# Optimization experiments

Measured on AMD Instinct MI355X. Metric: run time of the kernel, lower is better.

## Reference

```python
import jax, jax.numpy as jnp
import numpy as np

N_NODES = 16384
HID_IN = 1024   # hid_size (GCN in/out dim)
HID_MID = 1500  # hidden_size
N_EDGES = 131072


def setup_inputs() -> dict:
    key = jax.random.key(0)
    k1, k2, k3, k4, k5, k6 = jax.random.split(key, 6)
    x = jax.random.normal(k1, (N_NODES, HID_IN), dtype=jnp.float32)
    edge_index = jax.random.randint(k2, (2, N_EDGES), 0, N_NODES, dtype=jnp.int64)
    # GCNConv weights (glorot-ish scale) and biases
    W1 = jax.random.normal(k3, (HID_IN, HID_MID), dtype=jnp.float32) / np.sqrt(HID_IN)
    b1 = jnp.zeros((HID_MID,), dtype=jnp.float32)
    W2 = jax.random.normal(k4, (HID_MID, HID_IN), dtype=jnp.float32) / np.sqrt(HID_MID)
    b2 = jnp.zeros((HID_IN,), dtype=jnp.float32)
    return {"x": x, "edge_index": edge_index, "W1": W1, "b1": b1, "W2": W2, "b2": b2}


def _gcn_conv(x, W, b, src, dst, inv_sqrt_deg, n_nodes):
    # PyG GCNConv: out[i] = sum_{(j->i)} d_j^{-1/2} d_i^{-1/2} (x W)[j] + b
    h = x @ W                                   # [N, out]
    norm = inv_sqrt_deg[src] * inv_sqrt_deg[dst]  # [E]
    msg = h[src] * norm[:, None]                 # gather + scale [E, out]
    out = jax.ops.segment_sum(msg, dst, num_segments=n_nodes)
    return out + b


def reference(x, edge_index, W1, b1, W2, b2):
    n = x.shape[0]
    # add self-loops (GCNConv default)
    loops = jnp.arange(n, dtype=edge_index.dtype)
    src = jnp.concatenate([edge_index[0], loops])
    dst = jnp.concatenate([edge_index[1], loops])
    deg = jax.ops.segment_sum(jnp.ones_like(dst, dtype=x.dtype), dst, num_segments=n)
    inv_sqrt_deg = jnp.where(deg > 0, jax.lax.rsqrt(jnp.maximum(deg, 1.0)), 0.0)
    h = _gcn_conv(x, W1, b1, src, dst, inv_sqrt_deg, n)
    h = jax.nn.relu(h)  # dropout skipped (eval mode)
    out = _gcn_conv(h, W2, b2, src, dst, inv_sqrt_deg, n)
    return out
```

## Files before the change

### kernel.cpp

```cpp
#include <hip/hip_runtime.h>
#include <cstdint>
#include <cstddef>

#define NN 16384
#define DIN 1024
#define DMID 1500
#define DMIDP 1536
#define NE 131072

typedef __bf16 bf16;
typedef __bf16 bf16x4 __attribute__((ext_vector_type(4)));
typedef __bf16 bf16x8 __attribute__((ext_vector_type(8)));
typedef float f32x4 __attribute__((ext_vector_type(4)));

#define GLOBAL_AS __attribute__((address_space(1)))
#define LDS_AS __attribute__((address_space(3)))

__device__ __forceinline__ void gload_lds16(const bf16* g, bf16* l) {
    __builtin_amdgcn_global_load_lds((GLOBAL_AS const unsigned int*)(g),
                                     (LDS_AS unsigned int*)(l), 16, 0, 0);
}

#define SBAR() asm volatile("s_barrier" ::: "memory")
#define WAITV_(N) asm volatile("s_waitcnt vmcnt(" #N ")" ::: "memory")
#define WAITV(N) WAITV_(N)
#define WAITL0() asm volatile("s_waitcnt lgkmcnt(0)" ::: "memory")

__global__ void k_zero_cnt(int* cnt) {
    cnt[blockIdx.x * 256 + threadIdx.x] = 0;
}

__global__ void k_count(const int* __restrict__ dst, int* cnt) {
    int e = blockIdx.x * 256 + threadIdx.x;
    atomicAdd(&cnt[dst[e]], 1);
}

__global__ __launch_bounds__(1024) void k_scan(const int* __restrict__ cnt,
                                               int* __restrict__ rowptr,
                                               int* __restrict__ cursor,
                                               float* __restrict__ isd) {
    __shared__ int sums[1024];
    int t = threadIdx.x;
    int base = t * 16;
    int v[16], p[16];
    int s = 0;
#pragma unroll
    for (int k = 0; k < 16; ++k) {
        v[k] = cnt[base + k];
        p[k] = (v[k] + 7) & ~7;
        s += p[k];
    }
    sums[t] = s;
    __syncthreads();
    for (int off = 1; off < 1024; off <<= 1) {
        int y = (t >= off) ? sums[t - off] : 0;
        __syncthreads();
        sums[t] += y;
        __syncthreads();
    }
    int run = sums[t] - s;
#pragma unroll
    for (int k = 0; k < 16; ++k) {
        rowptr[base + k] = run;
        cursor[base + k] = run;
        isd[base + k] = rsqrtf((float)(v[k] + 1));
        run += p[k];
    }
    if (t == 1023) rowptr[NN] = run;
}

__global__ void k_fill(const int* __restrict__ src, const int* __restrict__ dst,
                       int* cursor, const float* __restrict__ isd,
                       int* __restrict__ csr_src, float* __restrict__ csr_w) {
    int e = blockIdx.x * 256 + threadIdx.x;
    int s = src[e], d = dst[e];
    int pos = atomicAdd(&cursor[d], 1);
    csr_src[pos] = s;
    csr_w[pos] = isd[s] * isd[d];
}

__global__ void k_pad(const int* __restrict__ cnt, const int* __restrict__ rowptr,
                      int* __restrict__ csr_src, float* __restrict__ csr_w) {
    int i = blockIdx.x * 256 + threadIdx.x;
    int c = cnt[i];
    int p = (c + 7) & ~7;
    int base = rowptr[i];
    for (int q = c; q < p; ++q) {
        csr_src[base + q] = i;
        csr_w[base + q] = 0.0f;
    }
}

__global__ void k_cvt_x(const float4* __restrict__ x, bf16x4* __restrict__ xb) {
    int i = blockIdx.x * 256 + threadIdx.x;
    float4 v = x[i];
    bf16x4 o;
    o[0] = (bf16)v.x; o[1] = (bf16)v.y; o[2] = (bf16)v.z; o[3] = (bf16)v.w;
    xb[i] = o;
}

__global__ void k_cvt_w1(const float* __restrict__ W1, bf16* __restrict__ W1b) {
    int n = blockIdx.x;
    for (int k = threadIdx.x; k < DIN; k += 256)
        W1b[n * DIN + k] = (n < DMID) ? (bf16)W1[(size_t)k * DMID + n] : (bf16)0.0f;
}

__global__ void k_cvt_w2(const float* __restrict__ W2, bf16* __restrict__ W2b) {
    int n = blockIdx.x;
    for (int k = threadIdx.x; k < DMIDP; k += 256)
        W2b[n * DMIDP + k] = (k < DMID) ? (bf16)W2[(size_t)k * DIN + n] : (bf16)0.0f;
}

template <int K, int N, bool RELU_BIAS>
__global__ __launch_bounds__(512, 2) void gemm256(const bf16* __restrict__ A,
                                                  const bf16* __restrict__ Bt,
                                                  bf16* __restrict__ C,
                                                  const float* __restrict__ bias) {
    constexpr int NT = K / 64;
    __shared__ __align__(16) bf16 lds[2][2][256 * 64];
    const int tid = threadIdx.x;
    const int w = tid >> 6;
    const int lane = tid & 63;
    const int bm = blockIdx.x, bn = blockIdx.y;
    const int fr = lane & 15, fq = lane >> 4;
    const int wm = w >> 2;
    const int wn = w & 3;
    const int sx = fr & 7;

    const int lrow = lane >> 3;
    const int lslot = (lane & 7) ^ lrow;
    const bf16* gA = A + (size_t)(bm * 256 + w * 8 + lrow) * K + lslot * 8;
    const bf16* gB = Bt + (size_t)(bn * 256 + w * 8 + lrow) * K + lslot * 8;

    f32x4 acc[8][4];
#pragma unroll
    for (int i = 0; i < 8; ++i)
#pragma unroll
        for (int j = 0; j < 4; ++j) acc[i][j] = {0.f, 0.f, 0.f, 0.f};

#define STAGE(T, BUF)                                                          \
    do {                                                                       \
        const bf16* _ga = gA + (size_t)(T) * 64;                               \
        const bf16* _gb = gB + (size_t)(T) * 64;                               \
        bf16* _la = &lds[BUF][0][0] + w * 512;                                 \
        bf16* _lb = &lds[BUF][1][0] + w * 512;                                 \
        _Pragma("unroll") for (int r = 0; r < 4; ++r)                          \
            gload_lds16(_ga + (size_t)r * (64 * K), _la + r * 4096);           \
        _Pragma("unroll") for (int r = 0; r < 4; ++r)                          \
            gload_lds16(_gb + (size_t)r * (64 * K), _lb + r * 4096);           \
    } while (0)

#define LDA4(DST, BUF, MH, KS)                                                 \
    _Pragma("unroll") for (int mt = 0; mt < 4; ++mt) {                         \
        int row = wm * 128 + (MH) * 64 + mt * 16 + fr;                         \
        int sl = (((KS) << 2) | fq) ^ sx;                                      \
        DST[mt] = *(const bf16x8*)((const char*)&lds[BUF][0][0] +              \
                                   row * 128 + sl * 16);                       \
    }
#define LDB4(DST, BUF, KS)                                                     \
    _Pragma("unroll") for (int nt = 0; nt < 4; ++nt) {                         \
        int row = wn * 64 + nt * 16 + fr;                                      \
        int sl = (((KS) << 2) | fq) ^ sx;                                      \
        DST[nt] = *(const bf16x8*)((const char*)&lds[BUF][1][0] +              \
                                   row * 128 + sl * 16);                       \
    }
#define MFMA16(MH, AF, BF)                                                     \
    __builtin_amdgcn_s_setprio(1);                                             \
    _Pragma("unroll") for (int mt = 0; mt < 4; ++mt)                           \
    _Pragma("unroll") for (int nt = 0; nt < 4; ++nt)                           \
        acc[(MH) * 4 + mt][nt] = __builtin_amdgcn_mfma_f32_16x16x32_bf16(      \
            AF[mt], BF[nt], acc[(MH) * 4 + mt][nt], 0, 0, 0);                  \
    __builtin_amdgcn_s_setprio(0);

    bf16x8 a0[4], a1[4], b0[4], b1[4];

    STAGE(0, 0);
    STAGE(1, 1);
    WAITV(8);
    SBAR();
    LDA4(a0, 0, 0, 0);
    LDB4(b0, 0, 0);

    for (int t = 0; t < NT; ++t) {
        const int b = t & 1;
        LDA4(a1, b, 1, 0);
        MFMA16(0, a0, b0);
        LDA4(a0, b, 0, 1);
        LDB4(b1, b, 1);
        MFMA16(1, a1, b0);
        LDA4(a1, b, 1, 1);
        MFMA16(0, a0, b1);
        if (t + 1 < NT) {
            WAITL0();
            WAITV(0);
            SBAR();
            if (t + 2 < NT) STAGE(t + 2, b);
            LDA4(a0, b ^ 1, 0, 0);
            LDB4(b0, b ^ 1, 0);
        }
        MFMA16(1, a1, b1);
    }
#undef STAGE
#undef LDA4
#undef LDB4
#undef MFMA16

    float bv[4];
    if (RELU_BIAS) {
#pragma unroll
        for (int nt = 0; nt < 4; ++nt) {
            int col = bn * 256 + wn * 64 + nt * 16 + fr;
            bv[nt] = (col < DMID) ? bias[col] : 0.0f;
        }
    }
#pragma unroll
    for (int mq = 0; mq < 8; ++mq) {
        int row0 = bm * 256 + wm * 128 + mq * 16 + fq * 4;
#pragma unroll
        for (int nt = 0; nt < 4; ++nt) {
            int col = bn * 256 + wn * 64 + nt * 16 + fr;
#pragma unroll
            for (int r = 0; r < 4; ++r) {
                float v = acc[mq][nt][r];
                if (RELU_BIAS) v = fmaxf(v + bv[nt], 0.0f);
                C[(size_t)(row0 + r) * N + col] = (bf16)v;
            }
        }
    }
}

__global__ __launch_bounds__(128) void k_aggX(const bf16* __restrict__ X,
                                              const int* __restrict__ rowptr,
                                              const int* __restrict__ csr_src,
                                              const float* __restrict__ csr_w,
                                              const float* __restrict__ isd,
                                              bf16* __restrict__ XA) {
    int i = blockIdx.x;
    int t = threadIdx.x;
    int c0 = t * 8;
    int beg = rowptr[i], end = rowptr[i + 1];
    float wi = isd[i];
    float w0 = wi * wi;
    float a[8];
    bf16x8 h = *(const bf16x8*)&X[(size_t)i * DIN + c0];
#pragma unroll
    for (int k = 0; k < 8; ++k) a[k] = w0 * (float)h[k];
    for (int e = beg; e < end; e += 8) {
        int j[8];
        float w[8];
        bf16x8 hv[8];
#pragma unroll
        for (int q = 0; q < 8; ++q) { j[q] = csr_src[e + q]; w[q] = csr_w[e + q]; }
#pragma unroll
        for (int q = 0; q < 8; ++q)
            hv[q] = *(const bf16x8*)&X[(size_t)j[q] * DIN + c0];
#pragma unroll
        for (int q = 0; q < 8; ++q)
#pragma unroll
            for (int k = 0; k < 8; ++k) a[k] += w[q] * (float)hv[q][k];
    }
    bf16x8 o;
#pragma unroll
    for (int k = 0; k < 8; ++k) o[k] = (bf16)a[k];
    *(bf16x8*)&XA[(size_t)i * DIN + c0] = o;
}

__global__ __launch_bounds__(128) void k_agg2(const bf16* __restrict__ H,
                                              const int* __restrict__ rowptr,
                                              const int* __restrict__ csr_src,
                                              const float* __restrict__ csr_w,
                                              const float* __restrict__ isd,
                                              const float* __restrict__ b2,
                                              float* __restrict__ out) {
    int i = blockIdx.x;
    int t = threadIdx.x;
    int c0 = t * 8;
    int beg = rowptr[i], end = rowptr[i + 1];
    float wi = isd[i];
    float w0 = wi * wi;
    float a[8];
    bf16x8 h = *(const bf16x8*)&H[(size_t)i * DIN + c0];
#pragma unroll
    for (int k = 0; k < 8; ++k) a[k] = w0 * (float)h[k];
    for (int e = beg; e < end; e += 8) {
        int j[8];
        float w[8];
        bf16x8 hv[8];
#pragma unroll
        for (int q = 0; q < 8; ++q) { j[q] = csr_src[e + q]; w[q] = csr_w[e + q]; }
#pragma unroll
        for (int q = 0; q < 8; ++q)
            hv[q] = *(const bf16x8*)&H[(size_t)j[q] * DIN + c0];
#pragma unroll
        for (int q = 0; q < 8; ++q)
#pragma unroll
            for (int k = 0; k < 8; ++k) a[k] += w[q] * (float)hv[q][k];
    }
    float4 o0, o1;
    o0.x = a[0] + b2[c0 + 0]; o0.y = a[1] + b2[c0 + 1];
    o0.z = a[2] + b2[c0 + 2]; o0.w = a[3] + b2[c0 + 3];
    o1.x = a[4] + b2[c0 + 4]; o1.y = a[5] + b2[c0 + 5];
    o1.z = a[6] + b2[c0 + 6]; o1.w = a[7] + b2[c0 + 7];
    *(float4*)&out[(size_t)i * DIN + c0] = o0;
    *(float4*)&out[(size_t)i * DIN + c0 + 4] = o1;
}

extern "C" void kernel_launch(void* const* d_in, const int* in_sizes, int n_in,
                              void* d_out, int out_size, void* d_ws, size_t ws_size,
                              hipStream_t stream) {
    const float* x = (const float*)d_in[0];
    const int* ei = (const int*)d_in[1];
    const float* W1 = (const float*)d_in[2];
    const float* b1 = (const float*)d_in[3];
    const float* W2 = (const float*)d_in[4];
    const float* b2 = (const float*)d_in[5];
    float* out = (float*)d_out;
    const int* src = ei;
    const int* dst = ei + NE;

    char* ws = (char*)d_ws;
    int* cnt      = (int*)(ws + 0);
    int* cursor   = (int*)(ws + 65536);
    float* isd    = (float*)(ws + 131072);
    int* rowptr   = (int*)(ws + 196608);
    int* csr_src  = (int*)(ws + 327680);
    float* csr_w  = (float*)(ws + 2424832);
    bf16* Xb      = (bf16*)(ws + 4521984);
    bf16* XA      = (bf16*)(ws + 38076416);
    bf16* W1b     = (bf16*)(ws + 71630848);
    bf16* W2b     = (bf16*)(ws + 74776576);
    bf16* Y1b     = (bf16*)(ws + 77922304);
    bf16* H2b     = XA;

    k_zero_cnt<<<NN / 256, 256, 0, stream>>>(cnt);
    k_count<<<NE / 256, 256, 0, stream>>>(dst, cnt);
    k_scan<<<1, 1024, 0, stream>>>(cnt, rowptr, cursor, isd);
    k_fill<<<NE / 256, 256, 0, stream>>>(src, dst, cursor, isd, csr_src, csr_w);
    k_pad<<<NN / 256, 256, 0, stream>>>(cnt, rowptr, csr_src, csr_w);

    k_cvt_x<<<NN * DIN / 4 / 256, 256, 0, stream>>>((const float4*)x, (bf16x4*)Xb);
    k_cvt_w1<<<DMIDP, 256, 0, stream>>>(W1, W1b);
    k_cvt_w2<<<DIN, 256, 0, stream>>>(W2, W2b);

    k_aggX<<<NN, 128, 0, stream>>>(Xb, rowptr, csr_src, csr_w, isd, XA);
    dim3 g1(NN / 256, DMIDP / 256);
    gemm256<DIN, DMIDP, true><<<g1, 512, 0, stream>>>(XA, W1b, Y1b, b1);

    dim3 g2(NN / 256, DIN / 256);
    gemm256<DMIDP, DIN, false><<<g2, 512, 0, stream>>>(Y1b, W2b, H2b, nullptr);
    k_agg2<<<NN, 128, 0, stream>>>(H2b, rowptr, csr_src, csr_w, isd, b2, out);
}
```

Before: 378.1 us.

## Parameterize GEMM M-tile, simplify K-loop, stage epilogue through LDS for vector stores

Templates the GEMM on M-tile size so the first GEMM uses 128-row tiles (more blocks for better CU fill) while the second keeps 256. The software-pipelined register double-buffering of fragments is replaced by a simpler per-k-step load-then-MFMA loop. The epilogue now writes accumulators into LDS and emits 16-byte coalesced global stores instead of scattered 2-byte stores. Risks are less LDS/MFMA overlap from the removed fragment prefetch and extra barriers in the epilogue.

Measured after the change: 509.5 us. 1.35x slower.

```diff
diff --git a/kernel.cpp b/kernel.cpp
--- a/kernel.cpp
+++ b/kernel.cpp
@@ -111,13 +111,19 @@
         W2b[n * DMIDP + k] = (k < DMID) ? (bf16)W2[(size_t)k * DIN + n] : (bf16)0.0f;
 }
 
-template <int K, int N, bool RELU_BIAS>
+template <int BM, int K, int N, bool RELU_BIAS>
 __global__ __launch_bounds__(512, 2) void gemm256(const bf16* __restrict__ A,
                                                   const bf16* __restrict__ Bt,
                                                   bf16* __restrict__ C,
                                                   const float* __restrict__ bias) {
+    static_assert(BM == 128 || BM == 256, "");
     constexpr int NT = K / 64;
-    __shared__ __align__(16) bf16 lds[2][2][256 * 64];
+    constexpr int WM = BM / 2;
+    constexpr int M_FR = WM / 16;
+    constexpr int AR = BM / 64;
+    constexpr int TOK = AR + 4;
+    __shared__ __align__(16) bf16 ldsA[2][BM * 64];
+    __shared__ __align__(16) bf16 ldsB[2][256 * 64];
     const int tid = threadIdx.x;
     const int w = tid >> 6;
     const int lane = tid & 63;
@@ -129,82 +135,74 @@
 
     const int lrow = lane >> 3;
     const int lslot = (lane & 7) ^ lrow;
-    const bf16* gA = A + (size_t)(bm * 256 + w * 8 + lrow) * K + lslot * 8;
-    const bf16* gB = Bt + (size_t)(bn * 256 + w * 8 + lrow) * K + lslot * 8;
-
-    f32x4 acc[8][4];
-#pragma unroll
-    for (int i = 0; i < 8; ++i)
+    const bf16* gA = A + (size_t)(bm * BM + w * 8 * AR + lrow) * K + lslot * 8;
+    const bf16* gB = Bt + (size_t)(bn * 256 + w * 32 + lrow) * K + lslot * 8;
+
+    f32x4 acc[M_FR][4];
+#pragma unroll
+    for (int i = 0; i < M_FR; ++i)
 #pragma unroll
         for (int j = 0; j < 4; ++j) acc[i][j] = {0.f, 0.f, 0.f, 0.f};
 
 #define STAGE(T, BUF)                                                          \
     do {                                                                       \
-        const bf16* _ga = gA + (size_t)(T) * 64;                               \
-        const bf16* _gb = gB + (size_t)(T) * 64;                               \
-        bf16* _la = &lds[BUF][0][0] + w * 512;                                 \
-        bf16* _lb = &lds[BUF][1][0] + w * 512;                                 \
+        _Pragma("unroll") for (int r = 0; r < AR; ++r)                         \
+            gload_lds16(gA + (size_t)(T) * 64 + (size_t)(r * 8) * K,           \
+                        &ldsA[BUF][0] + w * (AR * 512) + r * 512);             \
         _Pragma("unroll") for (int r = 0; r < 4; ++r)                          \
-            gload_lds16(_ga + (size_t)r * (64 * K), _la + r * 4096);           \
-        _Pragma("unroll") for (int r = 0; r < 4; ++r)                          \
-            gload_lds16(_gb + (size_t)r * (64 * K), _lb + r * 4096);           \
+            gload_lds16(gB + (size_t)(T) * 64 + (size_t)(r * 8) * K,           \
+                        &ldsB[BUF][0] + w * 2048 + r * 512);                   \
     } while (0)
-
-#define LDA4(DST, BUF, MH, KS)                                                 \
-    _Pragma("unroll") for (int mt = 0; mt < 4; ++mt) {                         \
-        int row = wm * 128 + (MH) * 64 + mt * 16 + fr;                         \
-        int sl = (((KS) << 2) | fq) ^ sx;                                      \
-        DST[mt] = *(const bf16x8*)((const char*)&lds[BUF][0][0] +              \
-                                   row * 128 + sl * 16);                       \
-    }
-#define LDB4(DST, BUF, KS)                                                     \
-    _Pragma("unroll") for (int nt = 0; nt < 4; ++nt) {                         \
-        int row = wn * 64 + nt * 16 + fr;                                      \
-        int sl = (((KS) << 2) | fq) ^ sx;                                      \
-        DST[nt] = *(const bf16x8*)((const char*)&lds[BUF][1][0] +              \
-                                   row * 128 + sl * 16);                       \
-    }
-#define MFMA16(MH, AF, BF)                                                     \
-    __builtin_amdgcn_s_setprio(1);                                             \
-    _Pragma("unroll") for (int mt = 0; mt < 4; ++mt)                           \
-    _Pragma("unroll") for (int nt = 0; nt < 4; ++nt)                           \
-        acc[(MH) * 4 + mt][nt] = __builtin_amdgcn_mfma_f32_16x16x32_bf16(      \
-            AF[mt], BF[nt], acc[(MH) * 4 + mt][nt], 0, 0, 0);                  \
-    __builtin_amdgcn_s_setprio(0);
-
-    bf16x8 a0[4], a1[4], b0[4], b1[4];
 
     STAGE(0, 0);
     STAGE(1, 1);
-    WAITV(8);
+    if constexpr (TOK == 6) { WAITV(6); } else { WAITV(8); }
     SBAR();
-    LDA4(a0, 0, 0, 0);
-    LDB4(b0, 0, 0);
 
     for (int t = 0; t < NT; ++t) {
-        const int b = t & 1;
-        LDA4(a1, b, 1, 0);
-        MFMA16(0, a0, b0);
-        LDA4(a0, b, 0, 1);
-        LDB4(b1, b, 1);
-        MFMA16(1, a1, b0);
-        LDA4(a1, b, 1, 1);
-        MFMA16(0, a0, b1);
+        const int c = t & 1;
+#pragma unroll
+        for (int ks = 0; ks < 2; ++ks) {
+            bf16x8 bq[4];
+#pragma unroll
+            for (int nt = 0; nt < 4; ++nt) {
+                int row = wn * 64 + nt * 16 + fr;
+                int sl = ((ks << 2) | fq) ^ sx;
+                bq[nt] = *(const bf16x8*)((const char*)&ldsB[c][0] +
+                                          row * 128 + sl * 16);
+            }
+#pragma unroll
+            for (int mh = 0; mh < M_FR / 4; ++mh) {
+                bf16x8 af[4];
+#pragma unroll
+                for (int mt = 0; mt < 4; ++mt) {
+                    int row = wm * WM + mh * 64 + mt * 16 + fr;
+                    int sl = ((ks << 2) | fq) ^ sx;
+                    af[mt] = *(const bf16x8*)((const char*)&ldsA[c][0] +
+                                              row * 128 + sl * 16);
+                }
+                __builtin_amdgcn_s_setprio(1);
+#pragma unroll
+                for (int mt = 0; mt < 4; ++mt)
+#pragma unroll
+                    for (int nt = 0; nt < 4; ++nt)
+                        acc[mh * 4 + mt][nt] =
+                            __builtin_amdgcn_mfma_f32_16x16x32_bf16(
+                                af[mt], bq[nt], acc[mh * 4 + mt][nt], 0, 0, 0);
+                __builtin_amdgcn_s_setprio(0);
+            }
+        }
         if (t + 1 < NT) {
             WAITL0();
             WAITV(0);
             SBAR();
-            if (t + 2 < NT) STAGE(t + 2, b);
-            LDA4(a0, b ^ 1, 0, 0);
-            LDB4(b0, b ^ 1, 0);
+            if (t + 2 < NT) STAGE(t + 2, c);
         }
-        MFMA16(1, a1, b1);
     }
 #undef STAGE
-#undef LDA4
-#undef LDB4
-#undef MFMA16
-
+
+    WAITL0();
+    SBAR();
     float bv[4];
     if (RELU_BIAS) {
 #pragma unroll
@@ -213,19 +211,28 @@
             bv[nt] = (col < DMID) ? bias[col] : 0.0f;
         }
     }
-#pragma unroll
-    for (int mq = 0; mq < 8; ++mq) {
-        int row0 = bm * 256 + wm * 128 + mq * 16 + fq * 4;
-#pragma unroll
-        for (int nt = 0; nt < 4; ++nt) {
-            int col = bn * 256 + wn * 64 + nt * 16 + fr;
+    constexpr int EP = 264;
+    bf16* ldsE = &ldsA[0][0];
+    const int erow = tid >> 4;
+    const int ecseg = tid & 15;
+#pragma unroll 1
+    for (int mt = 0; mt < M_FR; ++mt) {
+#pragma unroll
+        for (int nt = 0; nt < 4; ++nt)
 #pragma unroll
             for (int r = 0; r < 4; ++r) {
-                float v = acc[mq][nt][r];
+                float v = acc[mt][nt][r];
                 if (RELU_BIAS) v = fmaxf(v + bv[nt], 0.0f);
-                C[(size_t)(row0 + r) * N + col] = (bf16)v;
+                ldsE[(wm * 16 + fq * 4 + r) * EP + wn * 64 + nt * 16 + fr] =
+                    (bf16)v;
             }
-        }
+        __syncthreads();
+        bf16x8 v0 = *(const bf16x8*)&ldsE[erow * EP + ecseg * 16];
+        bf16x8 v1 = *(const bf16x8*)&ldsE[erow * EP + ecseg * 16 + 8];
+        size_t grow = (size_t)bm * BM + (erow >> 4) * WM + mt * 16 + (erow & 15);
+        *(bf16x8*)&C[grow * N + bn * 256 + ecseg * 16] = v0;
+        *(bf16x8*)&C[grow * N + bn * 256 + ecseg * 16 + 8] = v1;
+        __syncthreads();
     }
 }
 
@@ -343,10 +350,10 @@
     k_cvt_w2<<<DIN, 256, 0, stream>>>(W2, W2b);
 
     k_aggX<<<NN, 128, 0, stream>>>(Xb, rowptr, csr_src, csr_w, isd, XA);
-    dim3 g1(NN / 256, DMIDP / 256);
-    gemm256<DIN, DMIDP, true><<<g1, 512, 0, stream>>>(XA, W1b, Y1b, b1);
+    dim3 g1(NN / 128, DMIDP / 256);
+    gemm256<128, DIN, DMIDP, true><<<g1, 512, 0, stream>>>(XA, W1b, Y1b, b1);
 
     dim3 g2(NN / 256, DIN / 256);
-    gemm256<DMIDP, DIN, false><<<g2, 512, 0, stream>>>(Y1b, W2b, H2b, nullptr);
+    gemm256<256, DMIDP, DIN, false><<<g2, 512, 0, stream>>>(Y1b, W2b, H2b, nullptr);
     k_agg2<<<NN, 128, 0, stream>>>(H2b, rowptr, csr_src, csr_w, isd, b2, out);
 }
```
